# Kernel optimization log

Hardware: AMD Instinct MI355X
Metric: run time of the kernel (lower is better)

## Reference

```python
import jax, jax.numpy as jnp
import numpy as np

B, C, T, H, W = 8, 128, 16, 32, 32
M, N, CS = 64, 64, 64


def setup_inputs() -> dict:
    key = jax.random.key(0)
    ks = jax.random.split(key, 12)
    s = 0.02
    return {
        "input": jax.random.normal(ks[0], (B, C, T, H, W), dtype=jnp.float32),
        "condition": jax.random.normal(ks[1], (B, CS), dtype=jnp.float32),
        # 1x1x1 Conv3d weights collapse to (out, in) matrices
        "W_phi": jax.random.normal(ks[2], (M, C), dtype=jnp.float32) * s,
        "b_phi": jax.random.normal(ks[3], (M,), dtype=jnp.float32) * s,
        "W_theta": jax.random.normal(ks[4], (N, C), dtype=jnp.float32) * s,
        "b_theta": jax.random.normal(ks[5], (N,), dtype=jnp.float32) * s,
        "W_rho": jax.random.normal(ks[6], (N, C), dtype=jnp.float32) * s,
        "b_rho": jax.random.normal(ks[7], (N,), dtype=jnp.float32) * s,
        "W1": jax.random.normal(ks[8], (CS, CS), dtype=jnp.float32) * s,
        "b1": jax.random.normal(ks[9], (CS,), dtype=jnp.float32) * s,
        "W2": jax.random.normal(ks[10], (H * W, CS), dtype=jnp.float32) * s,
        "b2": jax.random.normal(ks[11], (H * W,), dtype=jnp.float32) * s,
    }


def _pointwise_conv3d(x, Wt, b):
    # Conv3d with kernel=1, stride=1 == channel mixing
    return jnp.einsum('bcthw,oc->bothw', x, Wt) + b[None, :, None, None, None]


def reference(input, condition, W_phi, b_phi, W_theta, b_theta, W_rho, b_rho, W1, b1, W2, b2):
    x = input.reshape(-1, C, T, H, W)
    cond = condition.reshape(x.shape[0], -1)
    A = _pointwise_conv3d(x, W_phi, b_phi)                       # (b,m,t,h,w)
    B0 = _pointwise_conv3d(x, W_theta, b_theta)                  # (b,n,t,h,w)
    Bm = jax.nn.softmax(B0.reshape(B0.shape[0], B0.shape[1], -1), axis=-1).reshape(B0.shape)
    # FC_Cond: Linear+ReLU, Linear+ReLU, then softmax over h*w
    h1 = jax.nn.relu(cond @ W1.T + b1)
    h2 = jax.nn.relu(h1 @ W2.T + b2)
    Cm = jax.nn.softmax(h2, axis=-1).reshape(-1, H, W)           # (b,h,w)
    BC = Bm * Cm[:, None, None, :, :]                            # (b,n,t,h,w)
    AB_T = jnp.einsum('bmthw,bnthw->bmn', A, BC)                 # (b,m,n)
    V = jax.nn.softmax(_pointwise_conv3d(x, W_rho, b_rho), axis=1)
    Z = jnp.einsum('bmn,bnthw->bmthw', AB_T, V)
    attn = jnp.transpose(Bm * V, (0, 1, 3, 4, 2))                # (b,n,h,w,t)
    return (Z, attn)
```

## Files before the change

kernel.cpp:

```cpp
#include <hip/hip_runtime.h>

#define CC 128
#define SB 16384

typedef _Float16 half2_t __attribute__((ext_vector_type(2)));
typedef _Float16 half4_t __attribute__((ext_vector_type(4)));
typedef _Float16 half8_t __attribute__((ext_vector_type(8)));
typedef float    f32x4  __attribute__((ext_vector_type(4)));

#define WH_OFF   0u
#define BIAS_OFF 49152u
#define CM_OFF   50176u
#define SUME_OFF 82944u
#define AB_OFF   86016u
#define PT_OFF   262144u
#define VT_OFF   33816576u

__global__ void k0_setup(const float* __restrict__ cond,
                         const float* __restrict__ W_phi, const float* __restrict__ b_phi,
                         const float* __restrict__ W_theta, const float* __restrict__ b_theta,
                         const float* __restrict__ W_rho, const float* __restrict__ b_rho,
                         const float* __restrict__ W1, const float* __restrict__ b1,
                         const float* __restrict__ W2, const float* __restrict__ b2,
                         char* __restrict__ wsc) {
  __shared__ float sc[64], sh1[64], red[256];
  int t = threadIdx.x, bid = blockIdx.x;
  if (bid < 8) {
    int b = bid;
    if (t < 64) sc[t] = cond[b*64 + t];
    __syncthreads();
    if (t < 64) {
      float acc = b1[t];
      for (int k = 0; k < 64; ++k) acc += sc[k] * W1[t*64 + k];
      sh1[t] = fmaxf(acc, 0.f);
    }
    __syncthreads();
    float ev[4]; float ps = 0.f;
    #pragma unroll
    for (int q = 0; q < 4; ++q) {
      int o = q*256 + t;
      float acc = b2[o];
      for (int k = 0; k < 64; ++k) acc += sh1[k] * W2[o*64 + k];
      ev[q] = __expf(fmaxf(acc, 0.f));
      ps += ev[q];
    }
    red[t] = ps; __syncthreads();
    for (int s = 128; s > 0; s >>= 1) { if (t < s) red[t] += red[t+s]; __syncthreads(); }
    float inv = 1.f / red[0];
    float* cm = (float*)(wsc + CM_OFF);
    #pragma unroll
    for (int q = 0; q < 4; ++q) cm[b*1024 + q*256 + t] = ev[q] * inv;
  } else {
    int r = bid - 8;
    _Float16* wh = (_Float16*)(wsc + WH_OFF);
    for (int i = r*256 + t; i < 24576; i += 2048) {
      int set = i >> 13, mk = i & 8191;
      const float* W = (set == 0) ? W_phi : (set == 1 ? W_theta : W_rho);
      wh[i] = (_Float16)W[mk];
    }
    float* ab = (float*)(wsc + AB_OFF);
    for (int i = r*256 + t; i < 32768; i += 2048) ab[i] = 0.f;
    if (r == 0 && t < 192) {
      float* bias = (float*)(wsc + BIAS_OFF);
      bias[t] = (t < 64) ? b_phi[t] : (t < 128 ? b_theta[t-64] : b_rho[t-128]);
    }
    if (r == 1) {
      float* se = (float*)(wsc + SUME_OFF);
      for (int i = t; i < 512; i += 256) se[i] = 0.f;
    }
  }
}

__global__ __launch_bounds__(512, 6) void kC_main(
    const float* __restrict__ x, const _Float16* __restrict__ wh,
    const float* __restrict__ bias, const float* __restrict__ cm,
    float* __restrict__ sumE, _Float16* __restrict__ vt,
    char* __restrict__ ptb,
    float* __restrict__ abf) {
  __shared__ char smem[35328];
  __shared__ float se_l[512];
  _Float16* Xh  = (_Float16*)smem;
  _Float16* A_l = (_Float16*)smem;
  _Float16* E_l = (_Float16*)(smem + 17408);

  int t = threadIdx.x;
  int lane = t & 63, wv = t >> 6, ln = lane & 15, q = lane >> 4;
  int bid = blockIdx.x, b = bid >> 7, chunk = bid & 127;
  int s0 = chunk * 128;

  const float* xb = x + (size_t)b*CC*SB + s0;
  #pragma unroll
  for (int r = 0; r < 8; ++r) {
    int fid = r*512 + t;
    int c = fid >> 5, s4 = (fid & 31) << 2;
    float4 v = *(const float4*)(xb + (size_t)c*SB + s4);
    half2_t p0 = { (_Float16)v.x, (_Float16)v.y };
    half2_t p1 = { (_Float16)v.z, (_Float16)v.w };
    *(half2_t*)&Xh[c*138 + s4]     = p0;
    *(half2_t*)&Xh[c*138 + s4 + 2] = p1;
  }
  __syncthreads();

  int myp = wv * 16;
  half8_t bf[4];
  #pragma unroll
  for (int kk = 0; kk < 4; ++kk) {
    half8_t h;
    #pragma unroll
    for (int j = 0; j < 8; ++j) h[j] = Xh[(kk*32 + q*8 + j)*138 + myp + ln];
    bf[kk] = h;
  }

  int gs = s0 + myp + ln;
  float cmv = cm[b*1024 + (gs & 1023)];
  __syncthreads();

  half8_t af[4][4];
  f32x4 d[4];

  auto conv = [&](int setoff) {
    #pragma unroll
    for (int mt = 0; mt < 4; ++mt)
      #pragma unroll
      for (int kk = 0; kk < 4; ++kk)
        af[mt][kk] = *(const half8_t*)(wh + setoff + (mt*16 + ln)*128 + kk*32 + q*8);
    #pragma unroll
    for (int mt = 0; mt < 4; ++mt)
      d[mt] = (f32x4){0.f, 0.f, 0.f, 0.f};
    #pragma unroll
    for (int kk = 0; kk < 4; ++kk)
      #pragma unroll
      for (int mt = 0; mt < 4; ++mt)
        d[mt] = __builtin_amdgcn_mfma_f32_16x16x32_f16(af[mt][kk], bf[kk], d[mt], 0, 0, 0);
  };

  conv(0);
  #pragma unroll
  for (int mt = 0; mt < 4; ++mt) {
    float bv[4]; *(float4*)bv = *(const float4*)(bias + mt*16 + q*4);
    #pragma unroll
    for (int r = 0; r < 4; ++r)
      A_l[(mt*16 + q*4 + r)*136 + myp + ln] = (_Float16)(d[mt][r] + bv[r]);
  }

  conv(8192);
  float ev[4][4];
  #pragma unroll
  for (int mt = 0; mt < 4; ++mt) {
    float bv[4]; *(float4*)bv = *(const float4*)(bias + 64 + mt*16 + q*4);
    #pragma unroll
    for (int r = 0; r < 4; ++r) {
      float e = __expf(d[mt][r] + bv[r]);
      ev[mt][r] = e;
      E_l[(mt*16 + q*4 + r)*136 + myp + ln] = (_Float16)(e * cmv);
    }
    #pragma unroll
    for (int r = 0; r < 4; ++r) {
      float v = ev[mt][r];
      v += __shfl_xor(v, 1); v += __shfl_xor(v, 2);
      v += __shfl_xor(v, 4); v += __shfl_xor(v, 8);
      if (ln == 0) se_l[wv*64 + mt*16 + q*4 + r] = v;
    }
  }

  conv(16384);
  #pragma unroll
  for (int mt = 0; mt < 4; ++mt) {
    float bv[4]; *(float4*)bv = *(const float4*)(bias + 128 + mt*16 + q*4);
    #pragma unroll
    for (int r = 0; r < 4; ++r)
      d[mt][r] = __expf(d[mt][r] + bv[r]);
  }
  float cs = 0.f;
  #pragma unroll
  for (int mt = 0; mt < 4; ++mt)
    #pragma unroll
    for (int r = 0; r < 4; ++r) cs += d[mt][r];
  cs += __shfl_xor(cs, 16);
  cs += __shfl_xor(cs, 32);
  cs = 1.f / cs;
  {
    size_t grow = (size_t)b*SB + gs;
    _Float16* vrow = vt + grow*64;
    char* prow = ptb + grow*128;
    #pragma unroll
    for (int mt = 0; mt < 4; ++mt) {
      half4_t hv, hp;
      #pragma unroll
      for (int r = 0; r < 4; ++r) {
        float vv = d[mt][r] * cs;
        hv[r] = (_Float16)vv;
        hp[r] = (_Float16)(vv * ev[mt][r]);
      }
      *(half4_t*)(vrow + mt*16 + q*4) = hv;
      *(half4_t*)(prow + (size_t)(mt*16 + q*4)*2) = hp;
    }
  }
  __syncthreads();

  if (t < 64) {
    float ssum = 0.f;
    #pragma unroll
    for (int w = 0; w < 8; ++w) ssum += se_l[w*64 + t];
    atomicAdd(&sumE[b*64 + t], ssum);
  }

  int wm = wv & 3, nh = wv >> 2;
  f32x4 dab[2];
  dab[0] = (f32x4){0.f, 0.f, 0.f, 0.f};
  dab[1] = (f32x4){0.f, 0.f, 0.f, 0.f};
  #pragma unroll
  for (int kk = 0; kk < 4; ++kk) {
    half8_t aab = *(half8_t*)&A_l[(wm*16 + ln)*136 + kk*32 + q*8];
    #pragma unroll
    for (int nn = 0; nn < 2; ++nn) {
      half8_t bab = *(half8_t*)&E_l[((nh*2 + nn)*16 + ln)*136 + kk*32 + q*8];
      dab[nn] = __builtin_amdgcn_mfma_f32_16x16x32_f16(aab, bab, dab[nn], 0, 0, 0);
    }
  }
  float* ab = abf + b*4096;
  #pragma unroll
  for (int nn = 0; nn < 2; ++nn)
    #pragma unroll
    for (int r = 0; r < 4; ++r)
      atomicAdd(&ab[(wm*16 + q*4 + r)*64 + (nh*2 + nn)*16 + ln], dab[nn][r]);
}

__global__ __launch_bounds__(256) void k34(const float* __restrict__ abf,
                                           const _Float16* __restrict__ vt,
                                           const char* __restrict__ ptb,
                                           const float* __restrict__ sumE,
                                           float* __restrict__ out) {
  __shared__ _Float16 sm[256*72];
  int t = threadIdx.x;
  if (blockIdx.x < 512) {
    _Float16* Ah = sm;
    int lane = t & 63, wv = t >> 6, ln = lane & 15, q = lane >> 4;
    int bid = blockIdx.x, b = bid >> 6, chunk = bid & 63;
    int s0 = chunk * 256;
    const float* ab = abf + b*4096;
    const float* se = sumE + b*64;
    #pragma unroll
    for (int r = 0; r < 16; ++r) {
      int idx = r*256 + t;
      int m = idx >> 6, n = idx & 63;
      Ah[m*72 + n] = (_Float16)(ab[idx] * (1024.f / se[n]));
    }
    __syncthreads();
    half8_t a8[4][2];
    #pragma unroll
    for (int mt = 0; mt < 4; ++mt)
      #pragma unroll
      for (int kk = 0; kk < 2; ++kk)
        a8[mt][kk] = *(half8_t*)&Ah[(mt*16 + ln)*72 + kk*32 + q*8];
    int sw = s0 + wv*64;
    #pragma unroll
    for (int nt = 0; nt < 4; ++nt) {
      int sb = sw + nt*16 + ln;
      const _Float16* vrow = vt + ((size_t)b*SB + sb)*64;
      half8_t b8[2];
      b8[0] = *(const half8_t*)(vrow + q*8);
      b8[1] = *(const half8_t*)(vrow + 32 + q*8);
      f32x4 dz[4];
      #pragma unroll
      for (int mt = 0; mt < 4; ++mt) dz[mt] = (f32x4){0.f, 0.f, 0.f, 0.f};
      #pragma unroll
      for (int kk = 0; kk < 2; ++kk)
        #pragma unroll
        for (int mt = 0; mt < 4; ++mt)
          dz[mt] = __builtin_amdgcn_mfma_f32_16x16x32_f16(a8[mt][kk], b8[kk], dz[mt], 0, 0, 0);
      #pragma unroll
      for (int mt = 0; mt < 4; ++mt)
        #pragma unroll
        for (int r = 0; r < 4; ++r)
          out[((size_t)(b*64 + mt*16 + q*4 + r))*SB + sb] = dz[mt][r] * (1.f/1024.f);
    }
  } else {
    _Float16* P_l = sm;
    int bid = blockIdx.x - 512;
    int b = bid >> 6, hw0 = (bid & 63) * 16;
    int st = t >> 4, h = t & 15;
    int s = st*1024 + hw0 + h;
    const char* prow = ptb + ((size_t)b*SB + s)*128;
    #pragma unroll
    for (int c8 = 0; c8 < 8; ++c8)
      *(half8_t*)&P_l[t*72 + c8*8] = *(const half8_t*)(prow + c8*16);
    __syncthreads();
    int n = t >> 2, oc = t & 3;
    float ri = 1.f / sumE[b*64 + n];
    float* orow = out + 8388608 + (size_t)(b*64 + n)*SB + hw0*16;
    #pragma unroll
    for (int i = 0; i < 16; ++i) {
      int j = oc*64 + i*4;
      int hh = j >> 4, stb = j & 15;
      float w[4];
      #pragma unroll
      for (int r = 0; r < 4; ++r)
        w[r] = (float)P_l[((stb + r)*16 + hh)*72 + n] * ri;
      *(float4*)(orow + j) = *(float4*)w;
    }
  }
}

extern "C" void kernel_launch(void* const* d_in, const int* in_sizes, int n_in,
                              void* d_out, int out_size, void* d_ws, size_t ws_size,
                              hipStream_t stream) {
  const float* input   = (const float*)d_in[0];
  const float* cond    = (const float*)d_in[1];
  const float* W_phi   = (const float*)d_in[2];
  const float* b_phi   = (const float*)d_in[3];
  const float* W_theta = (const float*)d_in[4];
  const float* b_theta = (const float*)d_in[5];
  const float* W_rho   = (const float*)d_in[6];
  const float* b_rho   = (const float*)d_in[7];
  const float* W1      = (const float*)d_in[8];
  const float* b1      = (const float*)d_in[9];
  const float* W2      = (const float*)d_in[10];
  const float* b2      = (const float*)d_in[11];
  char* wsc = (char*)d_ws;
  float* out = (float*)d_out;

  const _Float16* wh = (const _Float16*)(wsc + WH_OFF);
  const float* bias = (const float*)(wsc + BIAS_OFF);
  const float* cmp  = (const float*)(wsc + CM_OFF);
  float* sumE  = (float*)(wsc + SUME_OFF);
  float* abf   = (float*)(wsc + AB_OFF);
  _Float16* vt = (_Float16*)(wsc + VT_OFF);

  hipLaunchKernelGGL(k0_setup, dim3(16), dim3(256), 0, stream,
                     cond, W_phi, b_phi, W_theta, b_theta, W_rho, b_rho,
                     W1, b1, W2, b2, wsc);
  hipLaunchKernelGGL(kC_main, dim3(1024), dim3(512), 0, stream,
                     input, wh, bias, cmp, sumE, vt, (char*)(wsc + PT_OFF), abf);
  hipLaunchKernelGGL(k34, dim3(1024), dim3(256), 0, stream,
                     abf, vt, (const char*)(wsc + PT_OFF), sumE, out);
}
```

Before: 227.7 us.

## Halve main-kernel block size to 64 spatial positions and restructure weight loads

The main conv kernel now processes 64 spatial positions per block with 256 threads instead of 128 with 512, doubling the grid to 2048 blocks and roughly halving LDS per block. The AB^T partial product is remapped so each wave owns a 16-row m-tile over all four n-tiles with K=64. The conv helper now loads weight fragments per m-tile just before use instead of holding all 16 fragments at once, which lowers register pressure. The aim is more resident blocks and better latency hiding, at the cost of twice as many atomic adds into the AB and sumE accumulators.

```diff
diff --git a/kernel.cpp b/kernel.cpp
--- a/kernel.cpp
+++ b/kernel.cpp
@@ -71,33 +71,33 @@
   }
 }
 
-__global__ __launch_bounds__(512, 6) void kC_main(
+__global__ __launch_bounds__(256, 4) void kC_main(
     const float* __restrict__ x, const _Float16* __restrict__ wh,
     const float* __restrict__ bias, const float* __restrict__ cm,
     float* __restrict__ sumE, _Float16* __restrict__ vt,
     char* __restrict__ ptb,
     float* __restrict__ abf) {
-  __shared__ char smem[35328];
-  __shared__ float se_l[512];
+  __shared__ char smem[18432];
+  __shared__ float se_l[256];
   _Float16* Xh  = (_Float16*)smem;
   _Float16* A_l = (_Float16*)smem;
-  _Float16* E_l = (_Float16*)(smem + 17408);
+  _Float16* E_l = (_Float16*)(smem + 9216);
 
   int t = threadIdx.x;
   int lane = t & 63, wv = t >> 6, ln = lane & 15, q = lane >> 4;
-  int bid = blockIdx.x, b = bid >> 7, chunk = bid & 127;
-  int s0 = chunk * 128;
+  int bid = blockIdx.x, b = bid >> 8, chunk = bid & 255;
+  int s0 = chunk * 64;
 
   const float* xb = x + (size_t)b*CC*SB + s0;
   #pragma unroll
   for (int r = 0; r < 8; ++r) {
-    int fid = r*512 + t;
-    int c = fid >> 5, s4 = (fid & 31) << 2;
+    int fid = r*256 + t;
+    int c = fid >> 4, s4 = (fid & 15) << 2;
     float4 v = *(const float4*)(xb + (size_t)c*SB + s4);
     half2_t p0 = { (_Float16)v.x, (_Float16)v.y };
     half2_t p1 = { (_Float16)v.z, (_Float16)v.w };
-    *(half2_t*)&Xh[c*138 + s4]     = p0;
-    *(half2_t*)&Xh[c*138 + s4 + 2] = p1;
+    *(half2_t*)&Xh[c*66 + s4]     = p0;
+    *(half2_t*)&Xh[c*66 + s4 + 2] = p1;
   }
   __syncthreads();
 
@@ -107,7 +107,7 @@
   for (int kk = 0; kk < 4; ++kk) {
     half8_t h;
     #pragma unroll
-    for (int j = 0; j < 8; ++j) h[j] = Xh[(kk*32 + q*8 + j)*138 + myp + ln];
+    for (int j = 0; j < 8; ++j) h[j] = Xh[(kk*32 + q*8 + j)*66 + myp + ln];
     bf[kk] = h;
   }
 
@@ -115,23 +115,24 @@
   float cmv = cm[b*1024 + (gs & 1023)];
   __syncthreads();
 
-  half8_t af[4][4];
   f32x4 d[4];
+  float ev[4][4];
 
   auto conv = [&](int setoff) {
     #pragma unroll
-    for (int mt = 0; mt < 4; ++mt)
-      #pragma unroll
-      for (int kk = 0; kk < 4; ++kk)
-        af[mt][kk] = *(const half8_t*)(wh + setoff + (mt*16 + ln)*128 + kk*32 + q*8);
-    #pragma unroll
-    for (int mt = 0; mt < 4; ++mt)
-      d[mt] = (f32x4){0.f, 0.f, 0.f, 0.f};
-    #pragma unroll
-    for (int kk = 0; kk < 4; ++kk)
-      #pragma unroll
-      for (int mt = 0; mt < 4; ++mt)
-        d[mt] = __builtin_amdgcn_mfma_f32_16x16x32_f16(af[mt][kk], bf[kk], d[mt], 0, 0, 0);
+    for (int mt = 0; mt < 4; ++mt) {
+      const _Float16* wp = wh + setoff + (mt*16 + ln)*128 + q*8;
+      half8_t a0 = *(const half8_t*)(wp);
+      half8_t a1 = *(const half8_t*)(wp + 32);
+      half8_t a2 = *(const half8_t*)(wp + 64);
+      half8_t a3 = *(const half8_t*)(wp + 96);
+      f32x4 acc = (f32x4){0.f, 0.f, 0.f, 0.f};
+      acc = __builtin_amdgcn_mfma_f32_16x16x32_f16(a0, bf[0], acc, 0, 0, 0);
+      acc = __builtin_amdgcn_mfma_f32_16x16x32_f16(a1, bf[1], acc, 0, 0, 0);
+      acc = __builtin_amdgcn_mfma_f32_16x16x32_f16(a2, bf[2], acc, 0, 0, 0);
+      acc = __builtin_amdgcn_mfma_f32_16x16x32_f16(a3, bf[3], acc, 0, 0, 0);
+      d[mt] = acc;
+    }
   };
 
   conv(0);
@@ -140,11 +141,10 @@
     float bv[4]; *(float4*)bv = *(const float4*)(bias + mt*16 + q*4);
     #pragma unroll
     for (int r = 0; r < 4; ++r)
-      A_l[(mt*16 + q*4 + r)*136 + myp + ln] = (_Float16)(d[mt][r] + bv[r]);
+      A_l[(mt*16 + q*4 + r)*72 + myp + ln] = (_Float16)(d[mt][r] + bv[r]);
   }
 
   conv(8192);
-  float ev[4][4];
   #pragma unroll
   for (int mt = 0; mt < 4; ++mt) {
     float bv[4]; *(float4*)bv = *(const float4*)(bias + 64 + mt*16 + q*4);
@@ -152,7 +152,7 @@
     for (int r = 0; r < 4; ++r) {
       float e = __expf(d[mt][r] + bv[r]);
       ev[mt][r] = e;
-      E_l[(mt*16 + q*4 + r)*136 + myp + ln] = (_Float16)(e * cmv);
+      E_l[(mt*16 + q*4 + r)*72 + myp + ln] = (_Float16)(e * cmv);
     }
     #pragma unroll
     for (int r = 0; r < 4; ++r) {
@@ -199,31 +199,28 @@
   __syncthreads();
 
   if (t < 64) {
-    float ssum = 0.f;
-    #pragma unroll
-    for (int w = 0; w < 8; ++w) ssum += se_l[w*64 + t];
+    float ssum = se_l[t] + se_l[64+t] + se_l[128+t] + se_l[192+t];
     atomicAdd(&sumE[b*64 + t], ssum);
   }
 
-  int wm = wv & 3, nh = wv >> 2;
-  f32x4 dab[2];
-  dab[0] = (f32x4){0.f, 0.f, 0.f, 0.f};
-  dab[1] = (f32x4){0.f, 0.f, 0.f, 0.f};
-  #pragma unroll
-  for (int kk = 0; kk < 4; ++kk) {
-    half8_t aab = *(half8_t*)&A_l[(wm*16 + ln)*136 + kk*32 + q*8];
-    #pragma unroll
-    for (int nn = 0; nn < 2; ++nn) {
-      half8_t bab = *(half8_t*)&E_l[((nh*2 + nn)*16 + ln)*136 + kk*32 + q*8];
-      dab[nn] = __builtin_amdgcn_mfma_f32_16x16x32_f16(aab, bab, dab[nn], 0, 0, 0);
+  f32x4 dab[4];
+  #pragma unroll
+  for (int n2 = 0; n2 < 4; ++n2) dab[n2] = (f32x4){0.f, 0.f, 0.f, 0.f};
+  #pragma unroll
+  for (int kk = 0; kk < 2; ++kk) {
+    half8_t aab = *(half8_t*)&A_l[(wv*16 + ln)*72 + kk*32 + q*8];
+    #pragma unroll
+    for (int n2 = 0; n2 < 4; ++n2) {
+      half8_t bab = *(half8_t*)&E_l[(n2*16 + ln)*72 + kk*32 + q*8];
+      dab[n2] = __builtin_amdgcn_mfma_f32_16x16x32_f16(aab, bab, dab[n2], 0, 0, 0);
     }
   }
   float* ab = abf + b*4096;
   #pragma unroll
-  for (int nn = 0; nn < 2; ++nn)
+  for (int n2 = 0; n2 < 4; ++n2)
     #pragma unroll
     for (int r = 0; r < 4; ++r)
-      atomicAdd(&ab[(wm*16 + q*4 + r)*64 + (nh*2 + nn)*16 + ln], dab[nn][r]);
+      atomicAdd(&ab[(wv*16 + q*4 + r)*64 + n2*16 + ln], dab[n2][r]);
 }
 
 __global__ __launch_bounds__(256) void k34(const float* __restrict__ abf,
@@ -330,7 +327,7 @@
   hipLaunchKernelGGL(k0_setup, dim3(16), dim3(256), 0, stream,
                      cond, W_phi, b_phi, W_theta, b_theta, W_rho, b_rho,
                      W1, b1, W2, b2, wsc);
-  hipLaunchKernelGGL(kC_main, dim3(1024), dim3(512), 0, stream,
+  hipLaunchKernelGGL(kC_main, dim3(2048), dim3(256), 0, stream,
                      input, wh, bias, cmp, sumE, vt, (char*)(wsc + PT_OFF), abf);
   hipLaunchKernelGGL(k34, dim3(1024), dim3(256), 0, stream,
                      abf, vt, (const char*)(wsc + PT_OFF), sumE, out);
```

Result: slower. 237.3 us (+4.2%).
